# Kernel tuning notes

Hardware: AMD Instinct MI355X
Metric: run time of the kernel (lower is better)

## Reference

```python
import jax, jax.numpy as jnp
import numpy as np

N_NODES = 50000
N_EDGES = 1_600_000
IN_DIM = 512
HIDDEN = 512
OUT_DIM = 128
K = 10
ALPHA = 0.1


def setup_inputs() -> dict:
    key = jax.random.key(0)
    ks = jax.random.split(key, 7)
    x = jax.random.normal(ks[0], (N_NODES, IN_DIM), dtype=jnp.float32)
    edge_index = jax.random.randint(ks[1], (2, N_EDGES), 0, N_NODES, dtype=jnp.int64)
    s_in = 1.0 / np.sqrt(IN_DIM)
    s_h = 1.0 / np.sqrt(HIDDEN)
    lin_in_w = jax.random.uniform(ks[2], (HIDDEN, IN_DIM), jnp.float32, -s_in, s_in)
    lin_in_b = jax.random.uniform(ks[3], (HIDDEN,), jnp.float32, -s_in, s_in)
    lin_out_w = jax.random.uniform(ks[4], (OUT_DIM, HIDDEN), jnp.float32, -s_h, s_h)
    lin_out_b = jax.random.uniform(ks[5], (OUT_DIM,), jnp.float32, -s_h, s_h)
    # GPR init: alpha*(1-alpha)^k, normalized
    w = np.array([ALPHA * (1 - ALPHA) ** k for k in range(K + 1)], dtype=np.float32)
    gpr_weights = jnp.asarray(w / w.sum())
    return {
        "x": x, "edge_index": edge_index,
        "lin_in_w": lin_in_w, "lin_in_b": lin_in_b,
        "lin_out_w": lin_out_w, "lin_out_b": lin_out_b,
        "gpr_weights": gpr_weights,
    }


def reference(x, edge_index, lin_in_w, lin_in_b, lin_out_w, lin_out_b, gpr_weights):
    n = x.shape[0]
    loops = jnp.arange(n, dtype=edge_index.dtype)
    row = jnp.concatenate([edge_index[0], loops])  # [E+n]
    col = jnp.concatenate([edge_index[1], loops])
    # degree over rows (edge_index_sl[0]), clamped to >=1
    deg = jax.ops.segment_sum(jnp.ones_like(row, dtype=x.dtype), row, num_segments=n)
    dis = jnp.clip(deg, 1.0) ** -0.5  # deg^-0.5, [n]

    h = jax.nn.relu(x @ lin_in_w.T + lin_in_b)  # [n, hidden] (dropout = identity in eval)
    w = jax.nn.softmax(gpr_weights)  # [K+1]

    def step(carry, wk):
        h_prop, acc = carry
        hs = h_prop * dis[:, None]
        h_prop = jax.ops.segment_sum(hs[col], row, num_segments=n) * dis[:, None]
        return (h_prop, acc + wk * h_prop), None

    (_, h_final), _ = jax.lax.scan(step, (h, w[0] * h), w[1:])
    return h_final @ lin_out_w.T + lin_out_b
```

## Files before the change

### kernel.cpp

```cpp
#include <hip/hip_runtime.h>


#define SLOTS 96
#define NB2   98
#define BCAP  18432
#define CHUNK 4096

typedef __attribute__((ext_vector_type(8))) short short8;
typedef __attribute__((ext_vector_type(4))) float f32x4;

__device__ inline ushort f2bf(float f) {
    uint x = __float_as_uint(f);
    return (ushort)((x + 0x7fffu + ((x >> 16) & 1u)) >> 16);
}
__device__ inline float bflo(uint u) { return __uint_as_float(u << 16); }
__device__ inline float bfhi(uint u) { return __uint_as_float(u & 0xffff0000u); }

__device__ __forceinline__ void glds16(const ushort* g, ushort* l) {
    __builtin_amdgcn_global_load_lds(
        (const __attribute__((address_space(1))) void*)g,
        (__attribute__((address_space(3))) void*)l, 16, 0, 0);
}

__global__ void init_kernel(int* __restrict__ gcur, int ngc,
                            ushort* __restrict__ yAll, size_t ystride, int zrow,
                            uint* __restrict__ cfill, int cfcnt, uint cfval) {
    const int gid = blockIdx.x * blockDim.x + threadIdx.x;
    const int stride = gridDim.x * blockDim.x;
    for (int i = gid; i < cfcnt; i += stride) cfill[i] = cfval;
    for (int i = gid; i < ngc; i += stride) gcur[i] = 0;
    for (int i = gid; i < 11 * 128; i += stride) {
        int k = i >> 7, d = i & 127;
        yAll[(size_t)k * ystride + (size_t)zrow * 128 + d] = 0;
    }
}

__global__ __launch_bounds__(512) void partition_kernel(
    const int* __restrict__ row, const int* __restrict__ col,
    int* __restrict__ gcur, uint* __restrict__ bbuf, int E) {
    __shared__ int cnt[128];
    __shared__ int base[128];
    __shared__ int gbase[128];
    __shared__ uint sbuf[CHUNK];
    const int tid = threadIdx.x;
    const int e0 = blockIdx.x * CHUNK;
    if (tid < 128) cnt[tid] = 0;
    __syncthreads();
    int myb[8]; int myp[8]; uint mye[8];
#pragma unroll
    for (int j = 0; j < 8; ++j) {
        int i = e0 + tid + j * 512;
        myb[j] = -1;
        if (i < E) {
            int r = row[i];
            int c = col[i];
            myb[j] = r >> 9;
            mye[j] = ((uint)(r & 511) << 16) | (uint)c;
            myp[j] = atomicAdd(&cnt[myb[j]], 1);
        }
    }
    __syncthreads();
    if (tid < 128) base[tid] = cnt[tid];
    __syncthreads();
    for (int off = 1; off < 128; off <<= 1) {
        int v = 0;
        if (tid < 128 && tid >= off) v = base[tid - off];
        __syncthreads();
        if (tid < 128) base[tid] += v;
        __syncthreads();
    }
    if (tid < 128) base[tid] -= cnt[tid];
    __syncthreads();
    if (tid < NB2 && cnt[tid] > 0) gbase[tid] = atomicAdd(&gcur[tid], cnt[tid]);
    __syncthreads();
#pragma unroll
    for (int j = 0; j < 8; ++j)
        if (myb[j] >= 0) sbuf[base[myb[j]] + myp[j]] = mye[j];
    __syncthreads();
    const int wv = tid >> 6, lane = tid & 63;
    for (int b = wv; b < NB2; b += 8) {
        const int len = cnt[b], src = base[b], dst = gbase[b];
        for (int i = lane; i < len; i += 64) {
            int d = dst + i;
            if (d < BCAP) bbuf[(size_t)b * BCAP + d] = sbuf[src + i];
        }
    }
}

__global__ __launch_bounds__(1024) void expand2_kernel(
    const int* __restrict__ gcur, const uint* __restrict__ bbuf,
    ushort* __restrict__ col_s, int* __restrict__ deg,
    float* __restrict__ dis, float* __restrict__ dis2, float* __restrict__ rdis,
    int n) {
    __shared__ int cur[128];
    const int b = blockIdx.x >> 2;
    const int q = blockIdx.x & 3;
    const int tid = threadIdx.x;
    if (tid < 128) cur[tid] = 0;
    __syncthreads();
    int cb = gcur[b];
    if (cb > BCAP) cb = BCAP;
    const size_t bb = (size_t)b * BCAP;
    const int rlo = q * 128, rhi = rlo + 128;
    for (int i = tid; i < cb; i += 1024) {
        uint e = bbuf[bb + i];
        int rl = (int)(e >> 16);
        if (rl >= rlo && rl < rhi) {
            int p = atomicAdd(&cur[rl - rlo], 1);
            if (p < SLOTS)
                col_s[((size_t)(b * 512 + rl)) * SLOTS + p] = (ushort)(e & 0xffffu);
        }
    }
    __syncthreads();
    if (tid < 128) {
        int r = b * 512 + rlo + tid;
        if (r < n) {
            int d = cur[tid];
            deg[r] = d;
            float fd = (float)(d + 1);
            float di = rsqrtf(fd);
            dis[r] = di;
            dis2[r] = di * di;
            rdis[r] = sqrtf(fd);
        }
    }
}

__global__ void cvt_all_kernel(const float* __restrict__ x,
                               const float* __restrict__ win,
                               const float* __restrict__ wout,
                               ushort* __restrict__ x_bf,
                               ushort* __restrict__ win_bf,
                               ushort* __restrict__ wout_bf,
                               int nx_src8, int nx8, int nw18, int nw28) {
    const int gid = blockIdx.x * blockDim.x + threadIdx.x;
    const int stride = gridDim.x * blockDim.x;
    const int tot = nx8 + nw18 + nw28;
    for (int i = gid; i < tot; i += stride) {
        const float* src;
        ushort* dst;
        int idx;
        if (i < nx8) {
            if (i >= nx_src8) {
                short8 z = (short8)0;
                *reinterpret_cast<short8*>(x_bf + (size_t)i * 8) = z;
                continue;
            }
            src = x; dst = x_bf; idx = i;
        } else if (i < nx8 + nw18) {
            src = win; dst = win_bf; idx = i - nx8;
        } else {
            src = wout; dst = wout_bf; idx = i - nx8 - nw18;
        }
        const float4* s = reinterpret_cast<const float4*>(src + (size_t)idx * 8);
        float4 a = s[0], b = s[1];
        short8 o;
        o[0] = (short)f2bf(a.x); o[1] = (short)f2bf(a.y);
        o[2] = (short)f2bf(a.z); o[3] = (short)f2bf(a.w);
        o[4] = (short)f2bf(b.x); o[5] = (short)f2bf(b.y);
        o[6] = (short)f2bf(b.z); o[7] = (short)f2bf(b.w);
        *reinterpret_cast<short8*>(dst + (size_t)idx * 8) = o;
    }
}

__global__ __launch_bounds__(512) void gemm1_kernel(
    const ushort* __restrict__ A, const ushort* __restrict__ B,
    const float* __restrict__ bias, ushort* __restrict__ outH, int M) {
    __shared__ __align__(16) ushort As[128 * 32];
    __shared__ __align__(16) ushort Bs[256 * 32];
    const int tid = threadIdx.x;
    const int lane = tid & 63;
    const int w = tid >> 6;
    const int wm = (w >> 2) * 64, wn = (w & 3) * 64;
    const int bm = blockIdx.y * 128, bn = blockIdx.x * 256;
    const int lrow = lane & 15, lk8 = (lane >> 4) * 8;

    f32x4 acc[4][4];
#pragma unroll
    for (int i = 0; i < 4; ++i)
#pragma unroll
        for (int j = 0; j < 4; ++j) acc[i][j] = (f32x4)(0.f);

    const int arow = 16 * w + (lane >> 2);
    const int acol = (lane & 3) * 8;
    const ushort* gA = A + (size_t)(bm + arow) * 512 + acol;
    const ushort* gB0 = B + (size_t)(bn + 32 * w + (lane >> 2)) * 512 + acol;
    const ushort* gB1 = gB0 + (size_t)16 * 512;
    ushort* lA = As + w * 512;
    ushort* lB0 = Bs + w * 1024;
    ushort* lB1 = Bs + w * 1024 + 512;

    for (int k0 = 0; k0 < 512; k0 += 32) {
        glds16(gA + k0, lA);
        glds16(gB0 + k0, lB0);
        glds16(gB1 + k0, lB1);
        __syncthreads();
        short8 af[4], bfr[4];
#pragma unroll
        for (int mf = 0; mf < 4; ++mf)
            af[mf] = *reinterpret_cast<const short8*>(As + (wm + mf * 16 + lrow) * 32 + lk8);
#pragma unroll
        for (int nf = 0; nf < 4; ++nf)
            bfr[nf] = *reinterpret_cast<const short8*>(Bs + (wn + nf * 16 + lrow) * 32 + lk8);
#pragma unroll
        for (int mf = 0; mf < 4; ++mf)
#pragma unroll
            for (int nf = 0; nf < 4; ++nf)
                acc[mf][nf] = __builtin_amdgcn_mfma_f32_16x16x32_bf16(af[mf], bfr[nf], acc[mf][nf], 0, 0, 0);
        __syncthreads();
    }

#pragma unroll
    for (int mf = 0; mf < 4; ++mf) {
#pragma unroll
        for (int nf = 0; nf < 4; ++nf) {
            const int col = bn + wn + nf * 16 + lrow;
#pragma unroll
            for (int r = 0; r < 4; ++r) {
                const int row = bm + wm + mf * 16 + (lane >> 4) * 4 + r;
                if (row < M) {
                    float v = fmaxf(acc[mf][nf][r] + bias[col], 0.f);
                    outH[(size_t)row * 512 + col] = f2bf(v);
                }
            }
        }
    }
}

__global__ __launch_bounds__(256) void gemm2_kernel(
    const ushort* __restrict__ A, const ushort* __restrict__ B,
    const float* __restrict__ dis, ushort* __restrict__ outY, int M) {
    __shared__ __align__(16) ushort As[128 * 32];
    __shared__ __align__(16) ushort Bs[128 * 32];
    const int tid = threadIdx.x;
    const int lane = tid & 63;
    const int w = tid >> 6;
    const int wm = (w >> 1) * 64, wn = (w & 1) * 64;
    const int bm = blockIdx.x * 128;
    const int lrow = lane & 15, lk8 = (lane >> 4) * 8;

    f32x4 acc[4][4];
#pragma unroll
    for (int i = 0; i < 4; ++i)
#pragma unroll
        for (int j = 0; j < 4; ++j) acc[i][j] = (f32x4)(0.f);

    const int sub = 32 * w + (lane >> 2);
    const int acol = (lane & 3) * 8;
    const ushort* gA0 = A + (size_t)(bm + sub) * 512 + acol;
    const ushort* gA1 = gA0 + (size_t)16 * 512;
    const ushort* gB0 = B + (size_t)sub * 512 + acol;
    const ushort* gB1 = gB0 + (size_t)16 * 512;
    ushort* lA0 = As + w * 1024;
    ushort* lA1 = As + w * 1024 + 512;
    ushort* lB0 = Bs + w * 1024;
    ushort* lB1 = Bs + w * 1024 + 512;

    for (int k0 = 0; k0 < 512; k0 += 32) {
        glds16(gA0 + k0, lA0);
        glds16(gA1 + k0, lA1);
        glds16(gB0 + k0, lB0);
        glds16(gB1 + k0, lB1);
        __syncthreads();
        short8 af[4], bfr[4];
#pragma unroll
        for (int mf = 0; mf < 4; ++mf)
            af[mf] = *reinterpret_cast<const short8*>(As + (wm + mf * 16 + lrow) * 32 + lk8);
#pragma unroll
        for (int nf = 0; nf < 4; ++nf)
            bfr[nf] = *reinterpret_cast<const short8*>(Bs + (wn + nf * 16 + lrow) * 32 + lk8);
#pragma unroll
        for (int mf = 0; mf < 4; ++mf)
#pragma unroll
            for (int nf = 0; nf < 4; ++nf)
                acc[mf][nf] = __builtin_amdgcn_mfma_f32_16x16x32_bf16(af[mf], bfr[nf], acc[mf][nf], 0, 0, 0);
        __syncthreads();
    }

#pragma unroll
    for (int mf = 0; mf < 4; ++mf) {
#pragma unroll
        for (int nf = 0; nf < 4; ++nf) {
            const int col = wn + nf * 16 + lrow;
#pragma unroll
            for (int r = 0; r < 4; ++r) {
                const int row = bm + wm + mf * 16 + (lane >> 4) * 4 + r;
                if (row < M)
                    outY[(size_t)row * 128 + col] = f2bf(dis[row] * acc[mf][nf][r]);
            }
        }
    }
}

__global__ __launch_bounds__(256) void spmm128_kernel(
    const int* __restrict__ deg, const ushort* __restrict__ col_s,
    const float* __restrict__ dis2,
    const ushort* __restrict__ y_old, ushort* __restrict__ y_new, int n) {
    int wid = (blockIdx.x * 256 + threadIdx.x) >> 6;
    if (wid >= n) return;
    wid = __builtin_amdgcn_readfirstlane(wid);
    const int lane = threadIdx.x & 63;
    int cnt = deg[wid];
    if (cnt > SLOTS) cnt = SLOTS;
    const int cnt16 = (cnt + 15) & ~15;
    const ushort* __restrict__ cp = col_s + (size_t)wid * SLOTS;
    const uint* __restrict__ Y = reinterpret_cast<const uint*>(y_old);
    float s0a = 0.f, s1a = 0.f, s0b = 0.f, s1b = 0.f;
    for (int t = 0; t < cnt16; t += 16) {
        int c[16];
        uint v[16];
#pragma unroll
        for (int j = 0; j < 16; ++j) c[j] = (int)cp[t + j];
#pragma unroll
        for (int j = 0; j < 16; ++j) v[j] = Y[(size_t)c[j] * 64 + lane];
#pragma unroll
        for (int j = 0; j < 16; ++j) {
            if (j & 1) { s0b += bflo(v[j]); s1b += bfhi(v[j]); }
            else       { s0a += bflo(v[j]); s1a += bfhi(v[j]); }
        }
    }
    const uint u = Y[(size_t)wid * 64 + lane];
    const float d2 = dis2[wid];
    const float y0 = d2 * (bflo(u) + (s0a + s0b));
    const float y1 = d2 * (bfhi(u) + (s1a + s1b));
    const uint pv = (uint)f2bf(y0) | ((uint)f2bf(y1) << 16);
    __builtin_nontemporal_store(pv, &reinterpret_cast<uint*>(y_new)[(size_t)wid * 64 + lane]);
}

__global__ __launch_bounds__(256) void finsum_kernel(
    const ushort* __restrict__ yAll, size_t ystride_dw,
    const float* __restrict__ gpr, const float* __restrict__ rdis,
    const float* __restrict__ bout, float* __restrict__ outp, int n) {
    __shared__ float w[11];
    if (threadIdx.x == 0) {
        float m = gpr[0];
        for (int i = 1; i < 11; ++i) m = fmaxf(m, gpr[i]);
        float e[11], s = 0.f;
        for (int i = 0; i < 11; ++i) { e[i] = expf(gpr[i] - m); s += e[i]; }
        float inv = 1.f / s;
        for (int i = 0; i < 11; ++i) w[i] = e[i] * inv;
    }
    __syncthreads();
    const int gid = blockIdx.x * 256 + threadIdx.x;
    if (gid >= n * 64) return;
    const int row = gid >> 6;
    const int lane = gid & 63;
    const uint* __restrict__ Y = reinterpret_cast<const uint*>(yAll);
    float s0 = 0.f, s1 = 0.f;
#pragma unroll
    for (int k = 0; k < 11; ++k) {
        const uint v = Y[k * ystride_dw + (size_t)row * 64 + lane];
        const float wk = w[k];
        s0 = fmaf(wk, bflo(v), s0);
        s1 = fmaf(wk, bfhi(v), s1);
    }
    const float r = rdis[row];
    float2 o;
    o.x = fmaf(s0, r, bout[lane * 2 + 0]);
    o.y = fmaf(s1, r, bout[lane * 2 + 1]);
    *reinterpret_cast<float2*>(outp + (size_t)row * 128 + lane * 2) = o;
}

extern "C" void kernel_launch(void* const* d_in, const int* in_sizes, int n_in,
                              void* d_out, int out_size, void* d_ws, size_t ws_size,
                              hipStream_t stream) {
    const float* x    = (const float*)d_in[0];
    const int*   ei   = (const int*)d_in[1];
    const float* win  = (const float*)d_in[2];
    const float* bin  = (const float*)d_in[3];
    const float* wout = (const float*)d_in[4];
    const float* bout = (const float*)d_in[5];
    const float* gpr  = (const float*)d_in[6];
    float* out = (float*)d_out;

    const int n = in_sizes[0] / 512;
    const int E = in_sizes[1] / 2;
    const int Mpad = ((n + 127) / 128) * 128;
    const int NPAD = NB2 * 512;

    char* ws = (char*)d_ws;
    size_t off = 0;
    auto take = [&](size_t bytes) -> char* {
        char* p = ws + off;
        off += (bytes + 511) & ~(size_t)511;
        return p;
    };
    int*    deg     = (int*)take((size_t)n * sizeof(int));
    float*  dis     = (float*)take((size_t)n * sizeof(float));
    float*  dis2    = (float*)take((size_t)n * sizeof(float));
    float*  rdis    = (float*)take((size_t)n * sizeof(float));
    int*    gcur    = (int*)take(128 * sizeof(int));
    uint*   bbuf    = (uint*)take((size_t)NB2 * BCAP * sizeof(uint));
    ushort* col_s   = (ushort*)take((size_t)NPAD * SLOTS * sizeof(ushort));
    ushort* x_bf    = (ushort*)take((size_t)Mpad * 512 * sizeof(ushort));
    ushort* win_bf  = (ushort*)take((size_t)512 * 512 * sizeof(ushort));
    ushort* wout_bf = (ushort*)take((size_t)128 * 512 * sizeof(ushort));
    ushort* h_bf    = (ushort*)take((size_t)Mpad * 512 * sizeof(ushort));
    const size_t ystride = (size_t)Mpad * 128;
    ushort* yAll    = (ushort*)take(11 * ystride * sizeof(ushort));

    const int* rowp = ei;
    const int* colp = ei + E;

    init_kernel<<<2048, 256, 0, stream>>>(gcur, 128, yAll, ystride, n,
                                          (uint*)col_s, NPAD * SLOTS / 2,
                                          ((uint)n << 16) | (uint)n);
    partition_kernel<<<(E + CHUNK - 1) / CHUNK, 512, 0, stream>>>(rowp, colp, gcur, bbuf, E);
    expand2_kernel<<<NB2 * 4, 1024, 0, stream>>>(gcur, bbuf, col_s, deg, dis, dis2, rdis, n);

    cvt_all_kernel<<<2048, 256, 0, stream>>>(x, win, wout, x_bf, win_bf, wout_bf,
                                             n * 64, Mpad * 64, 512 * 64, 128 * 64);

    dim3 g1(2, Mpad / 128);
    gemm1_kernel<<<g1, 512, 0, stream>>>(x_bf, win_bf, bin, h_bf, n);

    gemm2_kernel<<<Mpad / 128, 256, 0, stream>>>(h_bf, wout_bf, dis, yAll, n);

    const int spmm_blocks = (n + 3) / 4;
    for (int k = 1; k <= 10; ++k) {
        spmm128_kernel<<<spmm_blocks, 256, 0, stream>>>(
            deg, col_s, dis2, yAll + (size_t)(k - 1) * ystride, yAll + (size_t)k * ystride, n);
    }

    finsum_kernel<<<(n * 64 + 255) / 256, 256, 0, stream>>>(
        yAll, ystride / 2, gpr, rdis, bout, out, n);
}
```

Measured before the change: 645.2 us.

## Slice propagated features into 8 column slices to localize SpMM gathers

Stores the propagated 128-wide bf16 feature matrix as eight 16-column slices, each a contiguous [rows x 16] array. The SpMM kernel now assigns each block to one slice, with 8 lanes per row, and broadcasts neighbor indices via shuffles. The aim is to keep each slice's working set (about 1.6MB) resident in cache and so cut gather misses to HBM. The trade-off is that each block reloads the neighbor index lists once per slice, 8 times in total, and each gather moves only 32B.

```diff
diff --git a/kernel.cpp b/kernel.cpp
--- a/kernel.cpp
+++ b/kernel.cpp
@@ -23,15 +23,17 @@
 }
 
 __global__ void init_kernel(int* __restrict__ gcur, int ngc,
-                            ushort* __restrict__ yAll, size_t ystride, int zrow,
+                            uint* __restrict__ yAll, size_t ystride32,
+                            size_t ss32, int zrow,
                             uint* __restrict__ cfill, int cfcnt, uint cfval) {
     const int gid = blockIdx.x * blockDim.x + threadIdx.x;
     const int stride = gridDim.x * blockDim.x;
     for (int i = gid; i < cfcnt; i += stride) cfill[i] = cfval;
     for (int i = gid; i < ngc; i += stride) gcur[i] = 0;
-    for (int i = gid; i < 11 * 128; i += stride) {
-        int k = i >> 7, d = i & 127;
-        yAll[(size_t)k * ystride + (size_t)zrow * 128 + d] = 0;
+    for (int i = gid; i < 11 * 8 * 8; i += stride) {
+        int k = i / 64, rem = i & 63;
+        int s = rem >> 3, f = rem & 7;
+        yAll[(size_t)k * ystride32 + (size_t)s * ss32 + (size_t)zrow * 8 + f] = 0;
     }
 }
 
@@ -229,7 +231,8 @@
 
 __global__ __launch_bounds__(256) void gemm2_kernel(
     const ushort* __restrict__ A, const ushort* __restrict__ B,
-    const float* __restrict__ dis, ushort* __restrict__ outY, int M) {
+    const float* __restrict__ dis, ushort* __restrict__ outY,
+    size_t ss16, int M) {
     __shared__ __align__(16) ushort As[128 * 32];
     __shared__ __align__(16) ushort Bs[128 * 32];
     const int tid = threadIdx.x;
@@ -282,62 +285,68 @@
 #pragma unroll
         for (int nf = 0; nf < 4; ++nf) {
             const int col = wn + nf * 16 + lrow;
+            const size_t sbase = (size_t)(col >> 4) * ss16 + (col & 15);
 #pragma unroll
             for (int r = 0; r < 4; ++r) {
                 const int row = bm + wm + mf * 16 + (lane >> 4) * 4 + r;
                 if (row < M)
-                    outY[(size_t)row * 128 + col] = f2bf(dis[row] * acc[mf][nf][r]);
+                    outY[sbase + (size_t)row * 16] = f2bf(dis[row] * acc[mf][nf][r]);
             }
         }
     }
 }
 
-__global__ __launch_bounds__(256) void spmm128_kernel(
+__global__ __launch_bounds__(256) void spmm_slice_kernel(
     const int* __restrict__ deg, const ushort* __restrict__ col_s,
     const float* __restrict__ dis2,
-    const ushort* __restrict__ y_old, ushort* __restrict__ y_new, int n) {
-    int wid = (blockIdx.x * 256 + threadIdx.x) >> 6;
-    if (wid >= n) return;
-    wid = __builtin_amdgcn_readfirstlane(wid);
+    const uint* __restrict__ y_old, uint* __restrict__ y_new,
+    size_t ss32, int n) {
+    const int s = blockIdx.x & 7;
+    const int grp = blockIdx.x >> 3;
     const int lane = threadIdx.x & 63;
-    int cnt = deg[wid];
+    const int wv = threadIdx.x >> 6;
+    const int r = grp * 32 + wv * 8 + (lane >> 3);
+    const int f = lane & 7;
+    if (r >= n) return;
+    const uint* __restrict__ Yo = y_old + (size_t)s * ss32;
+    int cnt = deg[r];
     if (cnt > SLOTS) cnt = SLOTS;
-    const int cnt16 = (cnt + 15) & ~15;
-    const ushort* __restrict__ cp = col_s + (size_t)wid * SLOTS;
-    const uint* __restrict__ Y = reinterpret_cast<const uint*>(y_old);
-    float s0a = 0.f, s1a = 0.f, s0b = 0.f, s1b = 0.f;
-    for (int t = 0; t < cnt16; t += 16) {
-        int c[16];
-        uint v[16];
-#pragma unroll
-        for (int j = 0; j < 16; ++j) c[j] = (int)cp[t + j];
-#pragma unroll
-        for (int j = 0; j < 16; ++j) v[j] = Y[(size_t)c[j] * 64 + lane];
-#pragma unroll
-        for (int j = 0; j < 16; ++j) {
-            if (j & 1) { s0b += bflo(v[j]); s1b += bfhi(v[j]); }
-            else       { s0a += bflo(v[j]); s1a += bfhi(v[j]); }
-        }
-    }
-    const uint u = Y[(size_t)wid * 64 + lane];
-    const float d2 = dis2[wid];
-    const float y0 = d2 * (bflo(u) + (s0a + s0b));
-    const float y1 = d2 * (bfhi(u) + (s1a + s1b));
-    const uint pv = (uint)f2bf(y0) | ((uint)f2bf(y1) << 16);
-    __builtin_nontemporal_store(pv, &reinterpret_cast<uint*>(y_new)[(size_t)wid * 64 + lane]);
+    const int cnt8 = (cnt + 7) & ~7;
+    const ushort* __restrict__ cp = col_s + (size_t)r * SLOTS;
+    float s0 = 0.f, s1 = 0.f, t0 = 0.f, t1 = 0.f;
+    for (int t = 0; t < cnt8; t += 8) {
+        const int myc = (int)__builtin_nontemporal_load(&cp[t + f]);
+        int c[8];
+        uint v[8];
+#pragma unroll
+        for (int j = 0; j < 8; ++j) c[j] = __shfl(myc, j, 8);
+#pragma unroll
+        for (int j = 0; j < 8; ++j) v[j] = Yo[(size_t)c[j] * 8 + f];
+#pragma unroll
+        for (int j = 0; j < 8; ++j) {
+            if (j & 1) { t0 += bflo(v[j]); t1 += bfhi(v[j]); }
+            else       { s0 += bflo(v[j]); s1 += bfhi(v[j]); }
+        }
+    }
+    const uint u = Yo[(size_t)r * 8 + f];
+    const float d2 = dis2[r];
+    const float y0 = d2 * (bflo(u) + (s0 + t0));
+    const float y1 = d2 * (bfhi(u) + (s1 + t1));
+    y_new[(size_t)s * ss32 + (size_t)r * 8 + f] =
+        (uint)f2bf(y0) | ((uint)f2bf(y1) << 16);
 }
 
 __global__ __launch_bounds__(256) void finsum_kernel(
-    const ushort* __restrict__ yAll, size_t ystride_dw,
+    const uint* __restrict__ yAll, size_t ystride32, size_t ss32,
     const float* __restrict__ gpr, const float* __restrict__ rdis,
     const float* __restrict__ bout, float* __restrict__ outp, int n) {
     __shared__ float w[11];
     if (threadIdx.x == 0) {
         float m = gpr[0];
         for (int i = 1; i < 11; ++i) m = fmaxf(m, gpr[i]);
-        float e[11], s = 0.f;
-        for (int i = 0; i < 11; ++i) { e[i] = expf(gpr[i] - m); s += e[i]; }
-        float inv = 1.f / s;
+        float e[11], sum = 0.f;
+        for (int i = 0; i < 11; ++i) { e[i] = expf(gpr[i] - m); sum += e[i]; }
+        float inv = 1.f / sum;
         for (int i = 0; i < 11; ++i) w[i] = e[i] * inv;
     }
     __syncthreads();
@@ -345,20 +354,22 @@
     if (gid >= n * 64) return;
     const int row = gid >> 6;
     const int lane = gid & 63;
-    const uint* __restrict__ Y = reinterpret_cast<const uint*>(yAll);
+    const int s = lane >> 3, f = lane & 7;
+    const size_t base = (size_t)s * ss32 + (size_t)row * 8 + f;
     float s0 = 0.f, s1 = 0.f;
 #pragma unroll
     for (int k = 0; k < 11; ++k) {
-        const uint v = Y[k * ystride_dw + (size_t)row * 64 + lane];
+        const uint v = yAll[k * ystride32 + base];
         const float wk = w[k];
         s0 = fmaf(wk, bflo(v), s0);
         s1 = fmaf(wk, bfhi(v), s1);
     }
     const float r = rdis[row];
+    const int cc = s * 16 + f * 2;
     float2 o;
-    o.x = fmaf(s0, r, bout[lane * 2 + 0]);
-    o.y = fmaf(s1, r, bout[lane * 2 + 1]);
-    *reinterpret_cast<float2*>(outp + (size_t)row * 128 + lane * 2) = o;
+    o.x = fmaf(s0, r, bout[cc + 0]);
+    o.y = fmaf(s1, r, bout[cc + 1]);
+    *reinterpret_cast<float2*>(outp + (size_t)row * 128 + cc) = o;
 }
 
 extern "C" void kernel_launch(void* const* d_in, const int* in_sizes, int n_in,
@@ -377,6 +388,11 @@
     const int E = in_sizes[1] / 2;
     const int Mpad = ((n + 127) / 128) * 128;
     const int NPAD = NB2 * 512;
+    const int NROWP = ((n + 1) + 63) & ~63;
+    const size_t ss16 = (size_t)NROWP * 16;
+    const size_t ss32 = ss16 / 2;
+    const size_t ystride16 = 8 * ss16;
+    const size_t ystride32 = ystride16 / 2;
 
     char* ws = (char*)d_ws;
     size_t off = 0;
@@ -396,13 +412,12 @@
     ushort* win_bf  = (ushort*)take((size_t)512 * 512 * sizeof(ushort));
     ushort* wout_bf = (ushort*)take((size_t)128 * 512 * sizeof(ushort));
     ushort* h_bf    = (ushort*)take((size_t)Mpad * 512 * sizeof(ushort));
-    const size_t ystride = (size_t)Mpad * 128;
-    ushort* yAll    = (ushort*)take(11 * ystride * sizeof(ushort));
+    ushort* yAll    = (ushort*)take(11 * ystride16 * sizeof(ushort));
 
     const int* rowp = ei;
     const int* colp = ei + E;
 
-    init_kernel<<<2048, 256, 0, stream>>>(gcur, 128, yAll, ystride, n,
+    init_kernel<<<2048, 256, 0, stream>>>(gcur, 128, (uint*)yAll, ystride32, ss32, n,
                                           (uint*)col_s, NPAD * SLOTS / 2,
                                           ((uint)n << 16) | (uint)n);
     partition_kernel<<<(E + CHUNK - 1) / CHUNK, 512, 0, stream>>>(rowp, colp, gcur, bbuf, E);
@@ -414,14 +429,16 @@
     dim3 g1(2, Mpad / 128);
     gemm1_kernel<<<g1, 512, 0, stream>>>(x_bf, win_bf, bin, h_bf, n);
 
-    gemm2_kernel<<<Mpad / 128, 256, 0, stream>>>(h_bf, wout_bf, dis, yAll, n);
-
-    const int spmm_blocks = (n + 3) / 4;
+    gemm2_kernel<<<Mpad / 128, 256, 0, stream>>>(h_bf, wout_bf, dis, yAll, ss16, n);
+
+    const int ngrp = (n + 31) / 32;
     for (int k = 1; k <= 10; ++k) {
-        spmm128_kernel<<<spmm_blocks, 256, 0, stream>>>(
-            deg, col_s, dis2, yAll + (size_t)(k - 1) * ystride, yAll + (size_t)k * ystride, n);
+        spmm_slice_kernel<<<ngrp * 8, 256, 0, stream>>>(
+            deg, col_s, dis2,
+            (const uint*)yAll + (size_t)(k - 1) * ystride32,
+            (uint*)yAll + (size_t)k * ystride32, ss32, n);
     }
 
     finsum_kernel<<<(n * 64 + 255) / 256, 256, 0, stream>>>(
-        yAll, ystride / 2, gpr, rdis, bout, out, n);
-}
+        (const uint*)yAll, ystride32, ss32, gpr, rdis, bout, out, n);
+}
```

Result: slower. 1.297 ms (+101.0%).
